# Performance work log

Hardware: AMD Instinct MI355X
Metric: run time of the kernel (lower is better)

Reference implementation:

```python
import jax, jax.numpy as jnp
import numpy as np

NUM_EMBEDDINGS = 1024
EMBEDDING_DIM = 64
COMMITMENT_COST = 0.25
EPS = 1e-12  # F.normalize clamp eps


def _l2_normalize(v):
    n = jnp.linalg.norm(v, axis=-1, keepdims=True)
    return v / jnp.maximum(n, EPS)


def setup_inputs() -> dict:
    key = jax.random.key(0)
    k_x, k_w = jax.random.split(key)
    x = jax.random.normal(k_x, (262144, EMBEDDING_DIM), dtype=jnp.float32)
    # nn.init.uniform_(weight, -1/K, 1/K)
    lim = 1.0 / NUM_EMBEDDINGS
    codebook = jax.random.uniform(k_w, (NUM_EMBEDDINGS, EMBEDDING_DIM),
                                  minval=-lim, maxval=lim, dtype=jnp.float32)
    return {"x": x, "codebook": codebook}


def reference(x, codebook):
    # Normalized vectors used only for nearest-neighbor search.
    xn = _l2_normalize(x)                      # [N, D]
    cn = _l2_normalize(codebook)               # [K, D]
    # ||xn||^2 + ||cn||^2 - 2 xn.cn  -> [N, K]
    distances = (jnp.sum(xn * xn, axis=1, keepdims=True)
                 + jnp.sum(cn * cn, axis=1)
                 - 2.0 * jnp.einsum('nd,kd->nk', xn, cn))
    encoding_indices = jnp.argmin(distances, axis=1)           # [N]
    quantized_unnormalized = codebook[encoding_indices]        # [N, D]
    sg = jax.lax.stop_gradient
    codebook_loss = jnp.mean((quantized_unnormalized - sg(x)) ** 2)
    commitment_loss = jnp.mean((x - sg(quantized_unnormalized)) ** 2)
    quantized_ste = x + sg(quantized_unnormalized - x)
    return quantized_ste, codebook_loss, commitment_loss, encoding_indices
```

## Files before the change

kernel.cpp:

```cpp
#include <hip/hip_runtime.h>
#include <math.h>

#define EPS 1e-12f
constexpr int N_ROWS = 262144;
constexpr int KCODES = 1024;
constexpr int DIM    = 64;
constexpr int CAP    = 65536;
constexpr int CHUNK_SH = 8192;
constexpr int TIE_THR = 15;

typedef __attribute__((ext_vector_type(8)))  short  short8;
typedef __attribute__((ext_vector_type(16))) float  float16;

__device__ inline unsigned short f2bf(float f) {
    unsigned int u = __float_as_uint(f);
    u = u + 0x7fff + ((u >> 16) & 1);
    return (unsigned short)(u >> 16);
}
__device__ inline float bf2f(unsigned short s) {
    return __uint_as_float(((unsigned int)s) << 16);
}

__global__ __launch_bounds__(64)
void vq_prep(const float* __restrict__ cb, float* __restrict__ cnT,
             float* __restrict__ cc, unsigned short* __restrict__ frag,
             int* __restrict__ cnt, float* __restrict__ dloss) {
    int n = blockIdx.x;
    int d = threadIdx.x;
    float v = cb[n * DIM + d];
    float s = v * v;
    #pragma unroll
    for (int off = 32; off; off >>= 1) s += __shfl_xor(s, off, 64);
    float vn = v / fmaxf(sqrtf(s), EPS);
    cnT[d * KCODES + n] = vn;
    float s2 = vn * vn;
    #pragma unroll
    for (int off = 32; off; off >>= 1) s2 += __shfl_xor(s2, off, 64);
    if (d == 0) cc[n] = s2;
    unsigned short hi = f2bf(vn);
    unsigned short lo = f2bf(vn - bf2f(hi));
    int c = n >> 7, t = (n >> 5) & 3;
    int lane = (n & 31) + 32 * ((d >> 3) & 1);
    int si = d >> 4, j = d & 7;
    size_t base = (size_t)(((c * 4 + t) * 4 + si) * 2) * 512 + lane * 8 + j;
    frag[base]       = hi;
    frag[base + 512] = lo;
    if (n == 0 && d == 0) { *cnt = 0; *dloss = 0.f; }
}

__global__ __launch_bounds__(256, 2)
void vq_mfma(const float* __restrict__ x, const unsigned short* __restrict__ frag,
             const float* __restrict__ cb, float* __restrict__ out_q,
             float* __restrict__ out_idx, int* __restrict__ cnt,
             int* __restrict__ list, float* __restrict__ partial) {
    __shared__ unsigned short Blds[2][CHUNK_SH];
    __shared__ int   ridx[128];
    __shared__ float redl[4];

    const int tid = threadIdx.x;
    const int w = tid >> 6, l = tid & 63;
    const int lc = l & 31, h = l >> 5;
    const int row0 = blockIdx.x * 128;

    short8 ahi[4], alo[4];
    {
        int row = row0 + w * 32 + lc;
        float xv[4][8]; float ss = 0.f;
        #pragma unroll
        for (int s = 0; s < 4; ++s) {
            const float* p = x + (size_t)row * DIM + s * 16 + h * 8;
            float4 a = *(const float4*)p;
            float4 b = *(const float4*)(p + 4);
            xv[s][0]=a.x; xv[s][1]=a.y; xv[s][2]=a.z; xv[s][3]=a.w;
            xv[s][4]=b.x; xv[s][5]=b.y; xv[s][6]=b.z; xv[s][7]=b.w;
            ss += a.x*a.x + a.y*a.y + a.z*a.z + a.w*a.w
                + b.x*b.x + b.y*b.y + b.z*b.z + b.w*b.w;
        }
        ss += __shfl_xor(ss, 32, 64);
        float inv = 1.0f / fmaxf(sqrtf(ss), EPS);
        #pragma unroll
        for (int s = 0; s < 4; ++s)
            #pragma unroll
            for (int j = 0; j < 8; ++j) {
                float v = xv[s][j] * inv;
                unsigned short hb = f2bf(v);
                unsigned short lb = f2bf(v - bf2f(hb));
                ahi[s][j] = (short)hb;
                alo[s][j] = (short)lb;
            }
    }

    int m1[16], m2[16];
    #pragma unroll
    for (int r = 0; r < 16; ++r) { m1[r] = 0; m2[r] = 0; }

    {
        const unsigned short* g = frag + (w * 4) * 512 + l * 8;
        #pragma unroll
        for (int q = 0; q < 4; ++q)
            __builtin_amdgcn_global_load_lds(
                (const __attribute__((address_space(1))) unsigned int*)(g + q * 512),
                (__attribute__((address_space(3))) unsigned int*)&Blds[0][(w * 4 + q) * 512],
                16, 0, 0);
    }

    for (int c = 0; c < 16; ++c) {
        __syncthreads();
        if (c < 15) {
            const unsigned short* g = frag + (size_t)(c + 1) * CHUNK_SH + (w * 4) * 512 + l * 8;
            #pragma unroll
            for (int q = 0; q < 4; ++q)
                __builtin_amdgcn_global_load_lds(
                    (const __attribute__((address_space(1))) unsigned int*)(g + q * 512),
                    (__attribute__((address_space(3))) unsigned int*)&Blds[(c + 1) & 1][(w * 4 + q) * 512],
                    16, 0, 0);
        }
        const unsigned short* B = Blds[c & 1];
        #pragma unroll
        for (int tt = 0; tt < 2; ++tt) {
            short8 bhi[4], blo[4];
            #pragma unroll
            for (int s = 0; s < 4; ++s) {
                bhi[s] = *((const short8*)&B[((tt * 4 + s) * 2    ) * 512] + l);
                blo[s] = *((const short8*)&B[((tt * 4 + s) * 2 + 1) * 512] + l);
            }
            int ct = c * 2 + tt;
            float16 acc;
            #pragma unroll
            for (int r = 0; r < 16; ++r) acc[r] = 2.0f;
            #pragma unroll
            for (int s = 0; s < 4; ++s) {
                acc = __builtin_amdgcn_mfma_f32_32x32x16_bf16(ahi[s], bhi[s], acc, 0, 0, 0);
                acc = __builtin_amdgcn_mfma_f32_32x32x16_bf16(alo[s], bhi[s], acc, 0, 0, 0);
                acc = __builtin_amdgcn_mfma_f32_32x32x16_bf16(ahi[s], blo[s], acc, 0, 0, 0);
            }
            #pragma unroll
            for (int r = 0; r < 16; ++r) {
                int k = (__float_as_int(acc[r]) & (int)0xFFFFFFE0) | ct;
                int nm2;
                asm("v_med3_i32 %0, %1, %2, %3"
                    : "=v"(nm2) : "v"(m1[r]), "v"(m2[r]), "v"(k));
                m2[r] = nm2;
                m1[r] = max(m1[r], k);
            }
        }
    }

    #pragma unroll
    for (int r = 0; r < 16; ++r) {
        int a = m1[r], b = m2[r];
        #pragma unroll
        for (int off = 1; off < 32; off <<= 1) {
            int oa = __shfl_xor(a, off, 64);
            int ob = __shfl_xor(b, off, 64);
            int nb = max(max(b, ob), min(a, oa));
            a = max(a, oa); b = nb;
        }
        unsigned long long ball = __ballot(m1[r] == a);
        unsigned m32 = h ? (unsigned)(ball >> 32) : (unsigned)ball;
        if (lc == 0) {
            int rowl = w * 32 + (r & 3) + 8 * (r >> 2) + 4 * h;
            int wlc = 31 - __builtin_clz(m32);
            ridx[rowl] = (a & 31) * 32 + wlc;
            if (((a >> 5) - (b >> 5)) <= TIE_THR) {
                int p = atomicAdd(cnt, 1);
                if (p < CAP) list[p] = row0 + rowl;
            }
        }
    }
    __syncthreads();

    if (tid < 128) out_idx[row0 + tid] = (float)ridx[tid];

    float lsum = 0.f;
    const float4* cb4 = (const float4*)cb;
    const float4* x4  = (const float4*)x;
    float4*       o4  = (float4*)out_q;
    #pragma unroll
    for (int i = 0; i < 8; ++i) {
        int f = tid + 256 * i;
        int r = f >> 4, c4 = f & 15;
        float4 q  = cb4[ridx[r] * 16 + c4];
        float4 xr = x4[(size_t)row0 * 16 + f];
        o4[(size_t)row0 * 16 + f] = q;
        float dx = q.x - xr.x, dy = q.y - xr.y, dz = q.z - xr.z, dw = q.w - xr.w;
        lsum += dx * dx + dy * dy + dz * dz + dw * dw;
    }
    #pragma unroll
    for (int off = 32; off; off >>= 1) lsum += __shfl_xor(lsum, off, 64);
    if (l == 0) redl[w] = lsum;
    __syncthreads();
    if (tid == 0) partial[blockIdx.x] = redl[0] + redl[1] + redl[2] + redl[3];
}

__global__ __launch_bounds__(256)
void vq_recheck(const float* __restrict__ x, const float* __restrict__ cnT,
                const float* __restrict__ cc, const float* __restrict__ cb,
                const int* __restrict__ cnt, const int* __restrict__ list,
                float* __restrict__ out_idx, float* __restrict__ out_q,
                float* __restrict__ dloss) {
    int w = threadIdx.x >> 6, l = threadIdx.x & 63;
    int wid = blockIdx.x * 4 + w, nw = gridDim.x * 4;
    int n = *cnt; if (n > CAP) n = CAP;
    for (int e = wid; e < n; e += nw) {
        int row = list[e];
        float xl = x[(size_t)row * DIM + l];
        float ss = xl * xl;
        #pragma unroll
        for (int off = 32; off; off >>= 1) ss += __shfl_xor(ss, off, 64);
        float inv = 1.0f / fmaxf(sqrtf(ss), EPS);
        float dot[16];
        #pragma unroll
        for (int kk = 0; kk < 16; ++kk) dot[kk] = 0.f;
        for (int d = 0; d < 64; ++d) {
            float xd = __shfl(xl, d, 64);
            #pragma unroll
            for (int kk = 0; kk < 16; ++kk)
                dot[kk] = fmaf(xd, cnT[d * KCODES + l + 64 * kk], dot[kk]);
        }
        float best = INFINITY; int bix = 0x7fffffff;
        #pragma unroll
        for (int kk = 0; kk < 16; ++kk) {
            int k = l + 64 * kk;
            float dist = cc[k] - 2.0f * (inv * dot[kk]);
            if (dist < best) { best = dist; bix = k; }
        }
        #pragma unroll
        for (int off = 1; off < 64; off <<= 1) {
            float ob = __shfl_xor(best, off, 64);
            int   oi = __shfl_xor(bix,  off, 64);
            if (ob < best || (ob == best && oi < bix)) { best = ob; bix = oi; }
        }
        int oldi = (int)out_idx[row];
        if (bix != oldi) {
            float qn = cb[(size_t)bix  * DIM + l];
            float qo = cb[(size_t)oldi * DIM + l];
            float an = qn - xl, ao = qo - xl;
            float dl = an * an - ao * ao;
            #pragma unroll
            for (int off = 32; off; off >>= 1) dl += __shfl_xor(dl, off, 64);
            out_q[(size_t)row * DIM + l] = qn;
            if (l == 0) { out_idx[row] = (float)bix; atomicAdd(dloss, dl); }
        }
    }
}

__global__ __launch_bounds__(256)
void vq_final(const float* __restrict__ partial, const float* __restrict__ dloss,
              float* __restrict__ out_loss) {
    float s = 0.f;
    for (int i = threadIdx.x; i < 2048; i += 256) s += partial[i];
    #pragma unroll
    for (int off = 32; off; off >>= 1) s += __shfl_xor(s, off, 64);
    __shared__ float red[4];
    if ((threadIdx.x & 63) == 0) red[threadIdx.x >> 6] = s;
    __syncthreads();
    if (threadIdx.x == 0) {
        float t = red[0] + red[1] + red[2] + red[3] + *dloss;
        float m = t / (float)((size_t)N_ROWS * DIM);
        out_loss[0] = m;
        out_loss[1] = m;
    }
}

extern "C" void kernel_launch(void* const* d_in, const int* in_sizes, int n_in,
                              void* d_out, int out_size, void* d_ws, size_t ws_size,
                              hipStream_t stream) {
    const float* x  = (const float*)d_in[0];
    const float* cb = (const float*)d_in[1];
    float* out = (float*)d_out;
    float* out_q    = out;
    float* out_loss = out + (size_t)N_ROWS * DIM;
    float* out_idx  = out_loss + 2;

    char* ws = (char*)d_ws;
    float*          cnT     = (float*)(ws);
    float*          cc      = (float*)(ws + 262144);
    unsigned short* frag    = (unsigned short*)(ws + 266240);
    int*            cnt     = (int*)(ws + 528384);
    float*          dloss   = (float*)(ws + 528388);
    int*            list    = (int*)(ws + 528400);
    float*          partial = (float*)(ws + 790544);

    vq_prep   <<<KCODES, 64, 0, stream>>>(cb, cnT, cc, frag, cnt, dloss);
    vq_mfma   <<<N_ROWS / 128, 256, 0, stream>>>(x, frag, cb, out_q, out_idx, cnt, list, partial);
    vq_recheck<<<512, 256, 0, stream>>>(x, cnT, cc, cb, cnt, list, out_idx, out_q, dloss);
    vq_final  <<<1, 256, 0, stream>>>(partial, dloss, out_loss);
}
```

Measured before the change: 226.4 us.

## Fuse tie recheck into MFMA kernel and halve LDS codebook chunk

Removes the separate recheck kernel and global atomic candidate list: each block keeps its near-tie rows in a shared-memory list and rechecks them in exact fp32 at the end of the main kernel, reading the old index from shared memory. The codebook chunk streamed through LDS is halved to 32 codes per iteration, with 32 iterations instead of 16 pairs of tiles. This saves a kernel launch and the global atomics, and cuts LDS use, which may help occupancy. The cost is twice as many barriers, and blocks with many tie rows now pay for the serial fp32 recheck inside the main kernel.

```diff
diff --git a/kernel.cpp b/kernel.cpp
--- a/kernel.cpp
+++ b/kernel.cpp
@@ -5,8 +5,7 @@
 constexpr int N_ROWS = 262144;
 constexpr int KCODES = 1024;
 constexpr int DIM    = 64;
-constexpr int CAP    = 65536;
-constexpr int CHUNK_SH = 8192;
+constexpr int CHUNK_SH = 4096;
 constexpr int TIE_THR = 15;
 
 typedef __attribute__((ext_vector_type(8)))  short  short8;
@@ -24,7 +23,7 @@
 __global__ __launch_bounds__(64)
 void vq_prep(const float* __restrict__ cb, float* __restrict__ cnT,
              float* __restrict__ cc, unsigned short* __restrict__ frag,
-             int* __restrict__ cnt, float* __restrict__ dloss) {
+             float* __restrict__ dloss) {
     int n = blockIdx.x;
     int d = threadIdx.x;
     float v = cb[n * DIM + d];
@@ -39,28 +38,33 @@
     if (d == 0) cc[n] = s2;
     unsigned short hi = f2bf(vn);
     unsigned short lo = f2bf(vn - bf2f(hi));
-    int c = n >> 7, t = (n >> 5) & 3;
+    int g = n >> 5;
     int lane = (n & 31) + 32 * ((d >> 3) & 1);
     int si = d >> 4, j = d & 7;
-    size_t base = (size_t)(((c * 4 + t) * 4 + si) * 2) * 512 + lane * 8 + j;
+    size_t base = (size_t)((g * 4 + si) * 2) * 512 + lane * 8 + j;
     frag[base]       = hi;
     frag[base + 512] = lo;
-    if (n == 0 && d == 0) { *cnt = 0; *dloss = 0.f; }
+    if (n == 0 && d == 0) *dloss = 0.f;
 }
 
 __global__ __launch_bounds__(256, 2)
 void vq_mfma(const float* __restrict__ x, const unsigned short* __restrict__ frag,
-             const float* __restrict__ cb, float* __restrict__ out_q,
-             float* __restrict__ out_idx, int* __restrict__ cnt,
-             int* __restrict__ list, float* __restrict__ partial) {
+             const float* __restrict__ cb, const float* __restrict__ cnT,
+             const float* __restrict__ cc, float* __restrict__ out_q,
+             float* __restrict__ out_idx, float* __restrict__ partial,
+             float* __restrict__ dloss) {
     __shared__ unsigned short Blds[2][CHUNK_SH];
     __shared__ int   ridx[128];
+    __shared__ int   blist[128];
+    __shared__ int   bcnt;
     __shared__ float redl[4];
 
     const int tid = threadIdx.x;
     const int w = tid >> 6, l = tid & 63;
     const int lc = l & 31, h = l >> 5;
     const int row0 = blockIdx.x * 128;
+
+    if (tid == 0) bcnt = 0;
 
     short8 ahi[4], alo[4];
     {
@@ -95,54 +99,50 @@
     for (int r = 0; r < 16; ++r) { m1[r] = 0; m2[r] = 0; }
 
     {
-        const unsigned short* g = frag + (w * 4) * 512 + l * 8;
-        #pragma unroll
-        for (int q = 0; q < 4; ++q)
+        const unsigned short* g = frag + (w * 2) * 512 + l * 8;
+        #pragma unroll
+        for (int q = 0; q < 2; ++q)
             __builtin_amdgcn_global_load_lds(
                 (const __attribute__((address_space(1))) unsigned int*)(g + q * 512),
-                (__attribute__((address_space(3))) unsigned int*)&Blds[0][(w * 4 + q) * 512],
+                (__attribute__((address_space(3))) unsigned int*)&Blds[0][(w * 2 + q) * 512],
                 16, 0, 0);
     }
 
-    for (int c = 0; c < 16; ++c) {
+    for (int c = 0; c < 32; ++c) {
         __syncthreads();
-        if (c < 15) {
-            const unsigned short* g = frag + (size_t)(c + 1) * CHUNK_SH + (w * 4) * 512 + l * 8;
-            #pragma unroll
-            for (int q = 0; q < 4; ++q)
+        if (c < 31) {
+            const unsigned short* g = frag + (size_t)(c + 1) * CHUNK_SH + (w * 2) * 512 + l * 8;
+            #pragma unroll
+            for (int q = 0; q < 2; ++q)
                 __builtin_amdgcn_global_load_lds(
                     (const __attribute__((address_space(1))) unsigned int*)(g + q * 512),
-                    (__attribute__((address_space(3))) unsigned int*)&Blds[(c + 1) & 1][(w * 4 + q) * 512],
+                    (__attribute__((address_space(3))) unsigned int*)&Blds[(c + 1) & 1][(w * 2 + q) * 512],
                     16, 0, 0);
         }
         const unsigned short* B = Blds[c & 1];
-        #pragma unroll
-        for (int tt = 0; tt < 2; ++tt) {
-            short8 bhi[4], blo[4];
-            #pragma unroll
-            for (int s = 0; s < 4; ++s) {
-                bhi[s] = *((const short8*)&B[((tt * 4 + s) * 2    ) * 512] + l);
-                blo[s] = *((const short8*)&B[((tt * 4 + s) * 2 + 1) * 512] + l);
-            }
-            int ct = c * 2 + tt;
-            float16 acc;
-            #pragma unroll
-            for (int r = 0; r < 16; ++r) acc[r] = 2.0f;
-            #pragma unroll
-            for (int s = 0; s < 4; ++s) {
-                acc = __builtin_amdgcn_mfma_f32_32x32x16_bf16(ahi[s], bhi[s], acc, 0, 0, 0);
-                acc = __builtin_amdgcn_mfma_f32_32x32x16_bf16(alo[s], bhi[s], acc, 0, 0, 0);
-                acc = __builtin_amdgcn_mfma_f32_32x32x16_bf16(ahi[s], blo[s], acc, 0, 0, 0);
-            }
-            #pragma unroll
-            for (int r = 0; r < 16; ++r) {
-                int k = (__float_as_int(acc[r]) & (int)0xFFFFFFE0) | ct;
-                int nm2;
-                asm("v_med3_i32 %0, %1, %2, %3"
-                    : "=v"(nm2) : "v"(m1[r]), "v"(m2[r]), "v"(k));
-                m2[r] = nm2;
-                m1[r] = max(m1[r], k);
-            }
+        short8 bhi[4], blo[4];
+        #pragma unroll
+        for (int s = 0; s < 4; ++s) {
+            bhi[s] = *((const short8*)&B[(s * 2    ) * 512] + l);
+            blo[s] = *((const short8*)&B[(s * 2 + 1) * 512] + l);
+        }
+        float16 acc;
+        #pragma unroll
+        for (int r = 0; r < 16; ++r) acc[r] = 2.0f;
+        #pragma unroll
+        for (int s = 0; s < 4; ++s) {
+            acc = __builtin_amdgcn_mfma_f32_32x32x16_bf16(ahi[s], bhi[s], acc, 0, 0, 0);
+            acc = __builtin_amdgcn_mfma_f32_32x32x16_bf16(alo[s], bhi[s], acc, 0, 0, 0);
+            acc = __builtin_amdgcn_mfma_f32_32x32x16_bf16(ahi[s], blo[s], acc, 0, 0, 0);
+        }
+        #pragma unroll
+        for (int r = 0; r < 16; ++r) {
+            int k = (__float_as_int(acc[r]) & (int)0xFFFFFFE0) | c;
+            int nm2;
+            asm("v_med3_i32 %0, %1, %2, %3"
+                : "=v"(nm2) : "v"(m1[r]), "v"(m2[r]), "v"(k));
+            m2[r] = nm2;
+            m1[r] = max(m1[r], k);
         }
     }
 
@@ -163,8 +163,8 @@
             int wlc = 31 - __builtin_clz(m32);
             ridx[rowl] = (a & 31) * 32 + wlc;
             if (((a >> 5) - (b >> 5)) <= TIE_THR) {
-                int p = atomicAdd(cnt, 1);
-                if (p < CAP) list[p] = row0 + rowl;
+                int p = atomicAdd(&bcnt, 1);
+                if (p < 128) blist[p] = rowl;
             }
         }
     }
@@ -191,19 +191,11 @@
     if (l == 0) redl[w] = lsum;
     __syncthreads();
     if (tid == 0) partial[blockIdx.x] = redl[0] + redl[1] + redl[2] + redl[3];
-}
-
-__global__ __launch_bounds__(256)
-void vq_recheck(const float* __restrict__ x, const float* __restrict__ cnT,
-                const float* __restrict__ cc, const float* __restrict__ cb,
-                const int* __restrict__ cnt, const int* __restrict__ list,
-                float* __restrict__ out_idx, float* __restrict__ out_q,
-                float* __restrict__ dloss) {
-    int w = threadIdx.x >> 6, l = threadIdx.x & 63;
-    int wid = blockIdx.x * 4 + w, nw = gridDim.x * 4;
-    int n = *cnt; if (n > CAP) n = CAP;
-    for (int e = wid; e < n; e += nw) {
-        int row = list[e];
+
+    int nfl = bcnt; if (nfl > 128) nfl = 128;
+    for (int e = w; e < nfl; e += 4) {
+        int rowl = blist[e];
+        int row  = row0 + rowl;
         float xl = x[(size_t)row * DIM + l];
         float ss = xl * xl;
         #pragma unroll
@@ -231,7 +223,7 @@
             int   oi = __shfl_xor(bix,  off, 64);
             if (ob < best || (ob == best && oi < bix)) { best = ob; bix = oi; }
         }
-        int oldi = (int)out_idx[row];
+        int oldi = ridx[rowl];
         if (bix != oldi) {
             float qn = cb[(size_t)bix  * DIM + l];
             float qo = cb[(size_t)oldi * DIM + l];
@@ -277,13 +269,11 @@
     float*          cnT     = (float*)(ws);
     float*          cc      = (float*)(ws + 262144);
     unsigned short* frag    = (unsigned short*)(ws + 266240);
-    int*            cnt     = (int*)(ws + 528384);
     float*          dloss   = (float*)(ws + 528388);
-    int*            list    = (int*)(ws + 528400);
     float*          partial = (float*)(ws + 790544);
 
-    vq_prep   <<<KCODES, 64, 0, stream>>>(cb, cnT, cc, frag, cnt, dloss);
-    vq_mfma   <<<N_ROWS / 128, 256, 0, stream>>>(x, frag, cb, out_q, out_idx, cnt, list, partial);
-    vq_recheck<<<512, 256, 0, stream>>>(x, cnT, cc, cb, cnt, list, out_idx, out_q, dloss);
-    vq_final  <<<1, 256, 0, stream>>>(partial, dloss, out_loss);
-}
+    vq_prep <<<KCODES, 64, 0, stream>>>(cb, cnT, cc, frag, dloss);
+    vq_mfma <<<N_ROWS / 128, 256, 0, stream>>>(x, frag, cb, cnT, cc,
+                                               out_q, out_idx, partial, dloss);
+    vq_final<<<1, 256, 0, stream>>>(partial, dloss, out_loss);
+}
```

Result: no change. 228.5 us (+1.0%).
